# Performance work log

Measured on AMD Instinct MI355X. Metric: run time of the kernel, lower is better.

## Reference

```python
import jax, jax.numpy as jnp
import numpy as np
from jax import lax
from jax.scipy.special import logsumexp

INSIZE = 256
NBASE = 4
SIZE = 2 * NBASE * (NBASE + 1)  # 40


def setup_inputs() -> dict:
    key = jax.random.key(0)
    kx, kw, kb = jax.random.split(key, 3)
    x = jax.random.normal(kx, (2048, 256, INSIZE), dtype=jnp.float32)
    W = jax.random.normal(kw, (SIZE, INSIZE), dtype=jnp.float32) / np.sqrt(INSIZE)
    b = 0.5 * jax.random.normal(kb, (SIZE,), dtype=jnp.float32)
    return {"x": x, "W": W, "b": b}


def global_norm_flipflop(scores):
    # scores: (T, N, C) with C = 2*nbase*(nbase+1)
    T, N, C = scores.shape
    nbase = int(np.sqrt(C / 2))
    assert 2 * nbase * (nbase + 1) == C

    fwd0 = jnp.zeros((N, 2 * nbase), dtype=scores.dtype)
    logZ0 = logsumexp(fwd0, axis=1, keepdims=True)  # (N, 1) = log(2*nbase)
    fwd0 = fwd0 - logZ0

    def step(carry, sc_t):
        fwd, logZ = carry
        # (N, nbase+1, 2*nbase): transition scores into each destination row
        sc = fwd[:, None, :] + sc_t.reshape(N, nbase + 1, 2 * nbase)
        base1 = logsumexp(sc[:, :nbase], axis=2)  # flip states (N, nbase)
        base2 = jnp.logaddexp(sc[:, nbase, :nbase], sc[:, nbase, nbase:])  # flop (N, nbase)
        new_state = jnp.concatenate([base1, base2], axis=1)  # (N, 2*nbase)
        factors = logsumexp(new_state, axis=1, keepdims=True)
        return (new_state - factors, logZ + factors), None

    (_, logZ), _ = lax.scan(step, (fwd0, logZ0), scores)
    return scores - logZ / T  # broadcast (N,1) over (T,N,C)


def reference(x, W, b):
    y = 5.0 * jnp.tanh(x @ W.T + b)  # (T, N, 40)
    return global_norm_flipflop(y)
```

## Files before the change

### kernel.cpp

```cpp
#include <hip/hip_runtime.h>
#include <hip/hip_bf16.h>

#define T_DIM 2048
#define N_DIM 256
#define K_DIM 256
#define C_DIM 40
#define CHUNK 32
#define NCHUNK 64
#define NT32 (T_DIM * N_DIM / 32)

#define LOG2E_F 1.44269504088896340736f
#define LN2_F   0.69314718055994530942f
#define NEGBIG  (-1.0e30f)

typedef short bf16x8 __attribute__((ext_vector_type(8)));
typedef float f32x4  __attribute__((ext_vector_type(4)));

__device__ __forceinline__ float fexp2(float x) { return exp2f(x); }
__device__ __forceinline__ float flog2(float x) { return log2f(x); }
__device__ __forceinline__ float frcp(float x) { return __frcp_rn(x); }

__device__ __forceinline__ unsigned int pk2(float a, float b)
{
    __hip_bfloat162 h = __float22bfloat162_rn(make_float2(a, b));
    unsigned int r;
    __builtin_memcpy(&r, &h, sizeof(r));
    return r;
}

__device__ __forceinline__ uint4 pack8u(float4 lo, float4 hi)
{
    uint4 t;
    t.x = pk2(lo.x, lo.y);
    t.y = pk2(lo.z, lo.w);
    t.z = pk2(hi.x, hi.y);
    t.w = pk2(hi.z, hi.w);
    return t;
}

__device__ __forceinline__ bf16x8 as_bf16x8(uint4 u)
{
    bf16x8 r;
    __builtin_memcpy(&r, &u, sizeof(r));
    return r;
}

__device__ __forceinline__ unsigned short bf16r(float v)
{
    return (unsigned short)(pk2(v, 0.0f) & 0xffffu);
}

__device__ __forceinline__ float bl(unsigned int w) { return __uint_as_float(w << 16); }
__device__ __forceinline__ float bh(unsigned int w) { return __uint_as_float(w & 0xffff0000u); }

__device__ __forceinline__ float tanh5(float v)
{
    const float e = fexp2(fabsf(v) * (2.0f * LOG2E_F));
    const float t = 1.0f - 2.0f * frcp(e + 1.0f);
    return 5.0f * copysignf(t, v);
}

__global__ __launch_bounds__(256, 2) void k1_gemm_tanh(
    const float* __restrict__ x, const float* __restrict__ W,
    const float* __restrict__ b, unsigned short* __restrict__ yb)
{
    __shared__ __align__(16) float xl[2][32 * 256];
    __shared__ __align__(16) float pl[2][12 * 64];

    const int tid  = threadIdx.x;
    const int wave = tid >> 6;
    const int lane = tid & 63;
    const int lr   = lane & 15;
    const int kg   = lane >> 4;
    const int mt   = wave & 1;
    const int kh   = wave >> 1;

    const float bc0 = b[lr];
    const float bc1 = b[16 + lr];
    const float bc2 = (lr < 8) ? b[32 + lr] : 0.0f;

    bf16x8 wf[4][3];
#pragma unroll
    for (int i = 0; i < 4; ++i) {
        const int ks = kh * 4 + i;
#pragma unroll
        for (int nt = 0; nt < 3; ++nt) {
            const int col = nt * 16 + lr;
            float4 lo = make_float4(0, 0, 0, 0), hi = lo;
            if (col < C_DIM) {
                const float* wp = W + (size_t)col * K_DIM + ks * 32 + kg * 8;
                lo = *(const float4*)wp;
                hi = *(const float4*)(wp + 4);
            }
            wf[i][nt] = as_bf16x8(pack8u(lo, hi));
        }
    }

#define STAGE(buf, st_)                                                        \
    {                                                                          \
        _Pragma("unroll")                                                      \
        for (int p = 0; p < 8; ++p) {                                          \
            const int r = wave * 8 + p;                                        \
            const float* gp = x + ((size_t)(st_) * 32 + r) * 256               \
                                + ((lane ^ (r & 7)) << 2);                     \
            __builtin_amdgcn_global_load_lds(                                  \
                (const __attribute__((address_space(1))) unsigned int*)gp,     \
                (__attribute__((address_space(3))) unsigned int*)&xl[buf][r * 256], \
                16, 0, 0);                                                     \
        }                                                                      \
    }

    const int rr = mt * 16 + lr;
    const int sw = lr & 7;

    int st = blockIdx.x;
    STAGE(0, st)
    asm volatile("s_waitcnt vmcnt(0)" ::: "memory");
    __builtin_amdgcn_s_barrier();

    int cur = 0;
#pragma unroll 1
    for (int t = 0; t < 32; ++t, st += 512) {
        if (t + 1 < 32) STAGE(cur ^ 1, st + 512)

        f32x4 af0, af1, af2;
        if (kh == 0) {
            af0 = (f32x4){bc0, bc0, bc0, bc0};
            af1 = (f32x4){bc1, bc1, bc1, bc1};
            af2 = (f32x4){bc2, bc2, bc2, bc2};
        } else {
            af0 = (f32x4){0.f, 0.f, 0.f, 0.f}; af1 = af0; af2 = af0;
        }
        const float* rowp = &xl[cur][rr * 256];
#pragma unroll
        for (int i = 0; i < 4; ++i) {
            const int u0 = (kh * 4 + i) * 8 + kg * 2;
            const float4 lo = *(const float4*)(rowp + ((u0 ^ sw) << 2));
            const float4 hi = *(const float4*)(rowp + (((u0 + 1) ^ sw) << 2));
            const bf16x8 a = as_bf16x8(pack8u(lo, hi));
            af0 = __builtin_amdgcn_mfma_f32_16x16x32_bf16(a, wf[i][0], af0, 0, 0, 0);
            af1 = __builtin_amdgcn_mfma_f32_16x16x32_bf16(a, wf[i][1], af1, 0, 0, 0);
            af2 = __builtin_amdgcn_mfma_f32_16x16x32_bf16(a, wf[i][2], af2, 0, 0, 0);
        }

        if (kh == 1) {
            float* p = &pl[mt][lane];
#pragma unroll
            for (int j = 0; j < 4; ++j) p[j * 64]       = af0[j];
#pragma unroll
            for (int j = 0; j < 4; ++j) p[(4 + j) * 64] = af1[j];
#pragma unroll
            for (int j = 0; j < 4; ++j) p[(8 + j) * 64] = af2[j];
        }
        asm volatile("s_waitcnt lgkmcnt(0)" ::: "memory");
        __builtin_amdgcn_s_barrier();

        if (kh == 0) {
            const float* p = &pl[mt][lane];
            unsigned short* yr =
                yb + ((size_t)st * 32 + mt * 16 + kg * 4) * C_DIM;
#pragma unroll
            for (int r = 0; r < 4; ++r) {
                yr[r * C_DIM + lr]      = bf16r(tanh5(af0[r] + p[r * 64]));
                yr[r * C_DIM + 16 + lr] = bf16r(tanh5(af1[r] + p[(4 + r) * 64]));
                if (lr < 8)
                    yr[r * C_DIM + 32 + lr] = bf16r(tanh5(af2[r] + p[(8 + r) * 64]));
            }
            asm volatile("s_waitcnt vmcnt(12)" ::: "memory");
        } else {
            asm volatile("s_waitcnt vmcnt(0)" ::: "memory");
        }
        __builtin_amdgcn_s_barrier();
        cur ^= 1;
    }
#undef STAGE
}

__global__ __launch_bounds__(256) void k2_chunks(
    const unsigned short* __restrict__ yb, float* __restrict__ cmat)
{
    const int tid  = threadIdx.x;
    const int wave = tid >> 6;
    const int lane = tid & 63;
    const int task = lane >> 3;
    const int c    = lane & 7;
    const int g    = blockIdx.x & (NCHUNK - 1);
    const int n    = ((blockIdx.x >> 6) << 5) + (wave << 3) + task;

    float col[8];
#pragma unroll
    for (int j = 0; j < 8; ++j) col[j] = (j == c) ? 0.0f : NEGBIG;

    const unsigned short* __restrict__ yp =
        yb + ((size_t)(g * CHUNK) * N_DIM + (size_t)n) * C_DIM;

#pragma unroll 1
    for (int s = 0; s < CHUNK; ++s) {
        float sc[C_DIM];
        const uint4* p4 = (const uint4*)yp;
#pragma unroll
        for (int q = 0; q < 5; ++q) {
            const uint4 u = p4[q];
            sc[8 * q + 0] = bl(u.x) * LOG2E_F;
            sc[8 * q + 1] = bh(u.x) * LOG2E_F;
            sc[8 * q + 2] = bl(u.y) * LOG2E_F;
            sc[8 * q + 3] = bh(u.y) * LOG2E_F;
            sc[8 * q + 4] = bl(u.z) * LOG2E_F;
            sc[8 * q + 5] = bh(u.z) * LOG2E_F;
            sc[8 * q + 6] = bl(u.w) * LOG2E_F;
            sc[8 * q + 7] = bh(u.w) * LOG2E_F;
        }
        float nc[8];
#pragma unroll
        for (int d = 0; d < 4; ++d) {
            float tv[8];
#pragma unroll
            for (int j = 0; j < 8; ++j) tv[j] = sc[d * 8 + j] + col[j];
            float m = tv[0];
#pragma unroll
            for (int j = 1; j < 8; ++j) m = fmaxf(m, tv[j]);
            float ss = 0.0f;
#pragma unroll
            for (int j = 0; j < 8; ++j) ss += fexp2(tv[j] - m);
            nc[d] = m + flog2(ss);
        }
#pragma unroll
        for (int i = 0; i < 4; ++i) {
            const float a  = sc[32 + i] + col[i];
            const float bb = sc[36 + i] + col[i + 4];
            const float m  = fmaxf(a, bb);
            const float ss = fexp2(a - m) + fexp2(bb - m);
            nc[4 + i] = m + flog2(ss);
        }
#pragma unroll
        for (int j = 0; j < 8; ++j) col[j] = nc[j];
        yp += (size_t)N_DIM * C_DIM;
    }
    float* __restrict__ op = cmat + (((size_t)g * 8 + c) * N_DIM + n) * 8;
#pragma unroll
    for (int j = 0; j < 8; ++j) op[j] = col[j];
}

__global__ __launch_bounds__(256) void k3_combine(
    const float* __restrict__ cmat, float* __restrict__ corr)
{
    const int tid = threadIdx.x;
    const int d   = tid & 7;
    const int n   = blockIdx.x * 32 + (tid >> 3);

    float v[8];
#pragma unroll
    for (int j = 0; j < 8; ++j) v[j] = 0.0f;

#pragma unroll 1
    for (int g = 0; g < NCHUNK; ++g) {
        const float* mg = cmat + ((size_t)g * 8 * N_DIM + n) * 8 + d;
        float mm[8];
#pragma unroll
        for (int j = 0; j < 8; ++j) mm[j] = mg[(size_t)j * N_DIM * 8];
        float tv[8];
#pragma unroll
        for (int j = 0; j < 8; ++j) tv[j] = mm[j] + v[j];
        float m = tv[0];
#pragma unroll
        for (int j = 1; j < 8; ++j) m = fmaxf(m, tv[j]);
        float ss = 0.0f;
#pragma unroll
        for (int j = 0; j < 8; ++j) ss += fexp2(tv[j] - m);
        const float nv = m + flog2(ss);
#pragma unroll
        for (int j = 0; j < 8; ++j) v[j] = __shfl(nv, j, 8);
    }
    float m = v[0];
#pragma unroll
    for (int j = 1; j < 8; ++j) m = fmaxf(m, v[j]);
    float ss = 0.0f;
#pragma unroll
    for (int j = 0; j < 8; ++j) ss += fexp2(v[j] - m);
    const float lz2 = m + flog2(ss);
    if (d == 0) corr[n] = lz2 * LN2_F / (float)T_DIM;
}

__global__ __launch_bounds__(256) void k4_final(
    const unsigned short* __restrict__ yb, const float* __restrict__ corr,
    float* __restrict__ out)
{
    const int i = blockIdx.x * 256 + threadIdx.x;
    const uint4 u = ((const uint4*)yb)[i];
    const float cr = corr[(i / 5) & (N_DIM - 1)];
    float4 o0, o1;
    o0.x = bl(u.x) - cr; o0.y = bh(u.x) - cr;
    o0.z = bl(u.y) - cr; o0.w = bh(u.y) - cr;
    o1.x = bl(u.z) - cr; o1.y = bh(u.z) - cr;
    o1.z = bl(u.w) - cr; o1.w = bh(u.w) - cr;
    float4* o4 = (float4*)out;
    o4[i * 2]     = o0;
    o4[i * 2 + 1] = o1;
}

extern "C" void kernel_launch(void* const* d_in, const int* in_sizes, int n_in,
                              void* d_out, int out_size, void* d_ws, size_t ws_size,
                              hipStream_t stream)
{
    const float* x = (const float*)d_in[0];
    const float* W = (const float*)d_in[1];
    const float* b = (const float*)d_in[2];
    float* out = (float*)d_out;

    unsigned short* ybf = (unsigned short*)d_ws;
    float* cmat = (float*)((char*)d_ws + (48u << 20));
    float* corr = cmat + (size_t)NCHUNK * 8 * N_DIM * 8;

    hipLaunchKernelGGL(k1_gemm_tanh, dim3(512),  dim3(256), 0, stream, x, W, b, ybf);
    hipLaunchKernelGGL(k2_chunks,    dim3(512),  dim3(256), 0, stream, ybf, cmat);
    hipLaunchKernelGGL(k3_combine,   dim3(8),    dim3(256), 0, stream, cmat, corr);
    hipLaunchKernelGGL(k4_final,     dim3(T_DIM * N_DIM * C_DIM / 8 / 256),
                       dim3(256), 0, stream, ybf, corr, out);
}
```

Before: 246.6 us.

## Halve k1 LDS staging per K-half and double chunk count for occupancy

```diff
diff --git a/kernel.cpp b/kernel.cpp
--- a/kernel.cpp
+++ b/kernel.cpp
@@ -5,8 +5,8 @@
 #define N_DIM 256
 #define K_DIM 256
 #define C_DIM 40
-#define CHUNK 32
-#define NCHUNK 64
+#define CHUNK 16
+#define NCHUNK 128
 #define NT32 (T_DIM * N_DIM / 32)
 
 #define LOG2E_F 1.44269504088896340736f
@@ -60,11 +60,11 @@
     return 5.0f * copysignf(t, v);
 }
 
-__global__ __launch_bounds__(256, 2) void k1_gemm_tanh(
+__global__ __launch_bounds__(256, 4) void k1_gemm_tanh(
     const float* __restrict__ x, const float* __restrict__ W,
     const float* __restrict__ b, unsigned short* __restrict__ yb)
 {
-    __shared__ __align__(16) float xl[2][32 * 256];
+    __shared__ __align__(16) float xl[2][32 * 128];
     __shared__ __align__(16) float pl[2][12 * 64];
 
     const int tid  = threadIdx.x;
@@ -73,39 +73,44 @@
     const int lr   = lane & 15;
     const int kg   = lane >> 4;
     const int mt   = wave & 1;
-    const int kh   = wave >> 1;
+    const int kq   = wave >> 1;
 
     const float bc0 = b[lr];
     const float bc1 = b[16 + lr];
     const float bc2 = (lr < 8) ? b[32 + lr] : 0.0f;
 
-    bf16x8 wf[4][3];
-#pragma unroll
-    for (int i = 0; i < 4; ++i) {
-        const int ks = kh * 4 + i;
-#pragma unroll
-        for (int nt = 0; nt < 3; ++nt) {
-            const int col = nt * 16 + lr;
-            float4 lo = make_float4(0, 0, 0, 0), hi = lo;
-            if (col < C_DIM) {
-                const float* wp = W + (size_t)col * K_DIM + ks * 32 + kg * 8;
-                lo = *(const float4*)wp;
-                hi = *(const float4*)(wp + 4);
+    bf16x8 wf[2][2][3];
+#pragma unroll
+    for (int h = 0; h < 2; ++h) {
+#pragma unroll
+        for (int i = 0; i < 2; ++i) {
+            const int ks = h * 4 + kq * 2 + i;
+#pragma unroll
+            for (int nt = 0; nt < 3; ++nt) {
+                const int col = nt * 16 + lr;
+                float4 lo = make_float4(0, 0, 0, 0), hi = lo;
+                if (col < C_DIM) {
+                    const float* wp = W + (size_t)col * K_DIM + ks * 32 + kg * 8;
+                    lo = *(const float4*)wp;
+                    hi = *(const float4*)(wp + 4);
+                }
+                wf[h][i][nt] = as_bf16x8(pack8u(lo, hi));
             }
-            wf[i][nt] = as_bf16x8(pack8u(lo, hi));
-        }
-    }
-
-#define STAGE(buf, st_)                                                        \
+        }
+    }
+
+#define STAGE(buf, st_, h_)                                                    \
     {                                                                          \
         _Pragma("unroll")                                                      \
-        for (int p = 0; p < 8; ++p) {                                          \
-            const int r = wave * 8 + p;                                        \
+        for (int p = 0; p < 4; ++p) {                                          \
+            const int rbase = wave * 8 + p * 2;                                \
+            const int r     = rbase + (lane >> 5);                             \
+            const int cu    = (lane & 31) ^ (r & 7);                           \
             const float* gp = x + ((size_t)(st_) * 32 + r) * 256               \
-                                + ((lane ^ (r & 7)) << 2);                     \
+                                + (h_) * 128 + (cu << 2);                      \
             __builtin_amdgcn_global_load_lds(                                  \
                 (const __attribute__((address_space(1))) unsigned int*)gp,     \
-                (__attribute__((address_space(3))) unsigned int*)&xl[buf][r * 256], \
+                (__attribute__((address_space(3))) unsigned int*)&xl[buf][rbase * 128], \
                 16, 0, 0);                                                     \
         }                                                                      \
     }
@@ -114,63 +119,77 @@
     const int sw = lr & 7;
 
     int st = blockIdx.x;
-    STAGE(0, st)
+    STAGE(0, st, 0)
     asm volatile("s_waitcnt vmcnt(0)" ::: "memory");
     __builtin_amdgcn_s_barrier();
 
+    f32x4 af0, af1, af2;
     int cur = 0;
 #pragma unroll 1
-    for (int t = 0; t < 32; ++t, st += 512) {
-        if (t + 1 < 32) STAGE(cur ^ 1, st + 512)
-
-        f32x4 af0, af1, af2;
-        if (kh == 0) {
-            af0 = (f32x4){bc0, bc0, bc0, bc0};
-            af1 = (f32x4){bc1, bc1, bc1, bc1};
-            af2 = (f32x4){bc2, bc2, bc2, bc2};
-        } else {
-            af0 = (f32x4){0.f, 0.f, 0.f, 0.f}; af1 = af0; af2 = af0;
-        }
-        const float* rowp = &xl[cur][rr * 256];
-#pragma unroll
-        for (int i = 0; i < 4; ++i) {
-            const int u0 = (kh * 4 + i) * 8 + kg * 2;
+    for (int t = 0; t < 32; ++t) {
+        const int h = t & 1;
+        if (t + 1 < 32) {
+            if (h == 0) STAGE(cur ^ 1, st, 1)
+            else        STAGE(cur ^ 1, st + 1024, 0)
+        }
+
+        if (h == 0) {
+            if (kq == 0) {
+                af0 = (f32x4){bc0, bc0, bc0, bc0};
+                af1 = (f32x4){bc1, bc1, bc1, bc1};
+                af2 = (f32x4){bc2, bc2, bc2, bc2};
+            } else {
+                af0 = (f32x4){0.f, 0.f, 0.f, 0.f}; af1 = af0; af2 = af0;
+            }
+        }
+
+        const float* rowp = &xl[cur][rr * 128];
+#pragma unroll
+        for (int i = 0; i < 2; ++i) {
+            const int u0 = (kq * 2 + i) * 8 + kg * 2;
             const float4 lo = *(const float4*)(rowp + ((u0 ^ sw) << 2));
             const float4 hi = *(const float4*)(rowp + (((u0 + 1) ^ sw) << 2));
             const bf16x8 a = as_bf16x8(pack8u(lo, hi));
-            af0 = __builtin_amdgcn_mfma_f32_16x16x32_bf16(a, wf[i][0], af0, 0, 0, 0);
-            af1 = __builtin_amdgcn_mfma_f32_16x16x32_bf16(a, wf[i][1], af1, 0, 0, 0);
-            af2 = __builtin_amdgcn_mfma_f32_16x16x32_bf16(a, wf[i][2], af2, 0, 0, 0);
-        }
-
-        if (kh == 1) {
-            float* p = &pl[mt][lane];
-#pragma unroll
-            for (int j = 0; j < 4; ++j) p[j * 64]       = af0[j];
-#pragma unroll
-            for (int j = 0; j < 4; ++j) p[(4 + j) * 64] = af1[j];
-#pragma unroll
-            for (int j = 0; j < 4; ++j) p[(8 + j) * 64] = af2[j];
-        }
-        asm volatile("s_waitcnt lgkmcnt(0)" ::: "memory");
-        __builtin_amdgcn_s_barrier();
-
-        if (kh == 0) {
-            const float* p = &pl[mt][lane];
-            unsigned short* yr =
-                yb + ((size_t)st * 32 + mt * 16 + kg * 4) * C_DIM;
-#pragma unroll
-            for (int r = 0; r < 4; ++r) {
-                yr[r * C_DIM + lr]      = bf16r(tanh5(af0[r] + p[r * 64]));
-                yr[r * C_DIM + 16 + lr] = bf16r(tanh5(af1[r] + p[(4 + r) * 64]));
-                if (lr < 8)
-                    yr[r * C_DIM + 32 + lr] = bf16r(tanh5(af2[r] + p[(8 + r) * 64]));
+            af0 = __builtin_amdgcn_mfma_f32_16x16x32_bf16(a, wf[h][i][0], af0, 0, 0, 0);
+            af1 = __builtin_amdgcn_mfma_f32_16x16x32_bf16(a, wf[h][i][1], af1, 0, 0, 0);
+            af2 = __builtin_amdgcn_mfma_f32_16x16x32_bf16(a, wf[h][i][2], af2, 0, 0, 0);
+        }
+
+        if (h == 1) {
+            if (kq == 1) {
+                float* p = &pl[mt][lane];
+#pragma unroll
+                for (int j = 0; j < 4; ++j) p[j * 64]       = af0[j];
+#pragma unroll
+                for (int j = 0; j < 4; ++j) p[(4 + j) * 64] = af1[j];
+#pragma unroll
+                for (int j = 0; j < 4; ++j) p[(8 + j) * 64] = af2[j];
             }
-            asm volatile("s_waitcnt vmcnt(12)" ::: "memory");
+            asm volatile("s_waitcnt lgkmcnt(0)" ::: "memory");
+            __builtin_amdgcn_s_barrier();
+
+            if (kq == 0) {
+                const float* p = &pl[mt][lane];
+                unsigned short* yr =
+                    yb + ((size_t)st * 32 + mt * 16 + kg * 4) * C_DIM;
+#pragma unroll
+                for (int r = 0; r < 4; ++r) {
+                    yr[r * C_DIM + lr]      = bf16r(tanh5(af0[r] + p[r * 64]));
+                    yr[r * C_DIM + 16 + lr] = bf16r(tanh5(af1[r] + p[(4 + r) * 64]));
+                    if (lr < 8)
+                        yr[r * C_DIM + 32 + lr] = bf16r(tanh5(af2[r] + p[(8 + r) * 64]));
+                }
+                asm volatile("s_waitcnt vmcnt(12)" ::: "memory");
+            } else {
+                asm volatile("s_waitcnt vmcnt(0)" ::: "memory");
+            }
+            __builtin_amdgcn_s_barrier();
+            st += 1024;
         } else {
+            asm volatile("s_waitcnt lgkmcnt(0)" ::: "memory");
             asm volatile("s_waitcnt vmcnt(0)" ::: "memory");
-        }
-        __builtin_amdgcn_s_barrier();
+            __builtin_amdgcn_s_barrier();
+        }
         cur ^= 1;
     }
 #undef STAGE
@@ -185,7 +204,7 @@
     const int task = lane >> 3;
     const int c    = lane & 7;
     const int g    = blockIdx.x & (NCHUNK - 1);
-    const int n    = ((blockIdx.x >> 6) << 5) + (wave << 3) + task;
+    const int n    = ((blockIdx.x >> 7) << 5) + (wave << 3) + task;
 
     float col[8];
 #pragma unroll
@@ -311,8 +330,8 @@
     float* cmat = (float*)((char*)d_ws + (48u << 20));
     float* corr = cmat + (size_t)NCHUNK * 8 * N_DIM * 8;
 
-    hipLaunchKernelGGL(k1_gemm_tanh, dim3(512),  dim3(256), 0, stream, x, W, b, ybf);
-    hipLaunchKernelGGL(k2_chunks,    dim3(512),  dim3(256), 0, stream, ybf, cmat);
+    hipLaunchKernelGGL(k1_gemm_tanh, dim3(1024), dim3(256), 0, stream, x, W, b, ybf);
+    hipLaunchKernelGGL(k2_chunks,    dim3(1024), dim3(256), 0, stream, ybf, cmat);
     hipLaunchKernelGGL(k3_combine,   dim3(8),    dim3(256), 0, stream, cmat, corr);
     hipLaunchKernelGGL(k4_final,     dim3(T_DIM * N_DIM * C_DIM / 8 / 256),
                        dim3(256), 0, stream, ybf, corr, out);
```

After: 367.0 us. +48.8%, slower.
